# Optimization experiments

Measured on AMD Instinct MI355X. Metric: run time of the kernel, lower is better.

The kernel has to match this reference:

```python
import jax, jax.numpy as jnp
import numpy as np

B, C, N, MAX_OUT = 8, 80, 8192, 100


def setup_inputs() -> dict:
    key = jax.random.key(0)
    k1, k2, k3 = jax.random.split(key, 3)
    xy = jax.random.uniform(k1, (B, N, 2), dtype=jnp.float32)          # top-left corners in [0,1)
    wh = jax.random.uniform(k2, (B, N, 2), dtype=jnp.float32,
                            minval=0.01, maxval=0.2)                    # realistic box sizes
    boxes = jnp.concatenate([xy, xy + wh], axis=-1)                     # [B,N,4] xyxy
    scores = jax.random.uniform(k3, (B, C, N), dtype=jnp.float32)       # [B,C,N]
    return {
        "boxes": boxes,
        "scores": scores,
        "max_output_boxes_per_class": MAX_OUT,
        "iou_threshold": jnp.array([0.5], dtype=jnp.float32),
        "score_threshold": jnp.array([0.5], dtype=jnp.float32),
    }


def _nms_single(boxes, scores, iou_thr, score_thr, max_out):
    """Greedy NMS for one (batch, class): boxes [N,4] xyxy, scores [N].
    Returns [max_out] selected box indices, padded with -1."""
    n = scores.shape[0]
    x1, y1, x2, y2 = boxes[:, 0], boxes[:, 1], boxes[:, 2], boxes[:, 3]
    area = jnp.maximum(x2 - x1, 0.0) * jnp.maximum(y2 - y1, 0.0)
    # score filtering (strictly greater, as in the torch module)
    s0 = jnp.where(scores > score_thr, scores, -jnp.inf)
    iota = jnp.arange(n)

    def body(s, _):
        i = jnp.argmax(s)
        valid = s[i] > -jnp.inf
        bx1, by1, bx2, by2 = boxes[i, 0], boxes[i, 1], boxes[i, 2], boxes[i, 3]
        iw = jnp.maximum(jnp.minimum(x2, bx2) - jnp.maximum(x1, bx1), 0.0)
        ih = jnp.maximum(jnp.minimum(y2, by2) - jnp.maximum(y1, by1), 0.0)
        inter = iw * ih
        union = area + area[i] - inter
        iou = jnp.where(union > 0, inter / union, 0.0)
        # suppress overlapping boxes (iou > thr keeps iou <= thr, matching torchvision.ops.nms)
        suppress = (iou > iou_thr) | (iota == i)
        s_new = jnp.where(suppress, -jnp.inf, s)
        s = jnp.where(valid, s_new, s)
        return s, jnp.where(valid, i, -1)

    _, idxs = jax.lax.scan(body, s0, None, length=max_out)
    return idxs  # [max_out] int32, -1 padded


def reference(boxes, scores, max_output_boxes_per_class, iou_threshold, score_threshold):
    max_out = int(max_output_boxes_per_class)
    iou_thr = iou_threshold[0]
    score_thr = score_threshold[0]
    b, c = scores.shape[0], scores.shape[1]

    # vmap over classes (boxes shared), then over batch
    per_batch = jax.vmap(
        lambda bb, ss: jax.vmap(
            lambda s: _nms_single(bb, s, iou_thr, score_thr, max_out)
        )(ss)
    )
    idxs = per_batch(boxes, scores)  # [B,C,max_out], -1 padded

    valid = idxs >= 0
    bidx = jnp.broadcast_to(jnp.arange(b)[:, None, None], idxs.shape)
    cidx = jnp.broadcast_to(jnp.arange(c)[None, :, None], idxs.shape)
    # [B*C*max_out, 3] rows of (batch, class, box_index); padded rows are (-1,-1,-1).
    triplets = jnp.stack(
        [jnp.where(valid, bidx, -1), jnp.where(valid, cidx, -1), idxs], axis=-1
    ).reshape(-1, 3).astype(jnp.int64)
    return triplets
```

## Files before the change

kernel.cpp:

```cpp
#include <hip/hip_runtime.h>
#include <math.h>
#include <stdint.h>

#define NMS_B 8
#define NMS_C 80
#define NMS_N 8192
#define NMS_MAX_OUT 100
#define BLOCK 512
#define PT 16
#define NBINS 256
#define TARGET 192
#define CAP 256
#define NW 4
#define PADROWS 8

__global__ __launch_bounds__(BLOCK) void nms_jacobi2_kernel(
    const float4* __restrict__ boxes,
    const float*  __restrict__ scores,
    const float*  __restrict__ iou_thr_p,
    const float*  __restrict__ score_thr_p,
    int32_t* __restrict__ out)
{
    const int bc   = blockIdx.x;
    const int b    = bc / NMS_C;
    const int c    = bc % NMS_C;
    const int t    = threadIdx.x;
    const int lane = t & 63;
    const int wv   = t >> 6;

    const float iou_thr   = *iou_thr_p;
    const float score_thr = *score_thr_p;

    __shared__ int      hist[NBINS];
    __shared__ int      cut_bin;
    __shared__ int      gcount;
    __shared__ alignas(16) uint64_t ckey[CAP];
    __shared__ float4   cbox[CAP];
    __shared__ int      cidx[CAP];
    __shared__ float4   sbox[CAP + PADROWS];
    __shared__ int      sidx[CAP];
    __shared__ alignas(16) uint64_t adjT[CAP * NW];

    if (t < NBINS) { hist[t] = 0; ckey[t] = 0; }
    for (int i = t; i < CAP + PADROWS; i += BLOCK)
        sbox[i] = make_float4(0.0f, 0.0f, 0.0f, 0.0f);
    if (t == 0) { cut_bin = 0; gcount = 0; }
    __syncthreads();

    const float* ss = scores + ((size_t)b * NMS_C + c) * NMS_N;
    const float4* ssv = (const float4*)ss;
    float s[PT];
    #pragma unroll
    for (int k4 = 0; k4 < PT / 4; ++k4) {
        float4 v = ssv[k4 * BLOCK + t];
        s[4 * k4 + 0] = v.x; s[4 * k4 + 1] = v.y;
        s[4 * k4 + 2] = v.z; s[4 * k4 + 3] = v.w;
    }
    const float inv_range =
        (score_thr < 1.0f) ? (float)NBINS / (1.0f - score_thr) : 0.0f;
    #pragma unroll
    for (int k = 0; k < PT; ++k) {
        if (s[k] > score_thr) {
            int bin = (int)((s[k] - score_thr) * inv_range);
            bin = bin > NBINS - 1 ? NBINS - 1 : bin;
            atomicAdd(&hist[bin], 1);
        }
    }
    __syncthreads();

    if (wv == 0) {
        int h0 = hist[lane], h1 = hist[64 + lane];
        int h2 = hist[128 + lane], h3 = hist[192 + lane];
        #pragma unroll
        for (int off = 1; off < 64; off <<= 1) {
            const int o0 = __shfl_down(h0, off);
            const int o1 = __shfl_down(h1, off);
            const int o2 = __shfl_down(h2, off);
            const int o3 = __shfl_down(h3, off);
            if (lane + off < 64) { h0 += o0; h1 += o1; h2 += o2; h3 += o3; }
        }
        const int tot1 = __shfl(h1, 0);
        const int tot2 = __shfl(h2, 0);
        const int tot3 = __shfl(h3, 0);
        const int S3 = h3;
        const int S2 = h2 + tot3;
        const int S1 = h1 + tot2 + tot3;
        const int S0 = h0 + tot1 + tot2 + tot3;
        const unsigned long long q3 = __ballot(S3 >= TARGET);
        const unsigned long long q2 = __ballot(S2 >= TARGET);
        const unsigned long long q1 = __ballot(S1 >= TARGET);
        const unsigned long long q0 = __ballot(S0 >= TARGET);
        int cut = 0;
        if      (q3) cut = 192 + 63 - __clzll(q3);
        else if (q2) cut = 128 + 63 - __clzll(q2);
        else if (q1) cut = 64  + 63 - __clzll(q1);
        else if (q0) cut = 63 - __clzll(q0);
        if (lane == 0) cut_bin = cut;
    }
    __syncthreads();
    const int cb = cut_bin;

    const float4* bb = boxes + (size_t)b * NMS_N;
    #pragma unroll
    for (int k = 0; k < PT; ++k) {
        if (s[k] > score_thr) {
            int bin = (int)((s[k] - score_thr) * inv_range);
            bin = bin > NBINS - 1 ? NBINS - 1 : bin;
            if (bin >= cb) {
                int pos = atomicAdd(&gcount, 1);
                if (pos < CAP) {
                    const int k4 = k >> 2, e = k & 3;
                    const int idx = (k4 * BLOCK + t) * 4 + e;
                    cbox[pos] = bb[idx];
                    cidx[pos] = idx;
                    ckey[pos] = ((uint64_t)__float_as_uint(s[k]) << 32) |
                                (uint32_t)(NMS_N - idx);
                }
            }
        }
    }
    __syncthreads();
    const int M = gcount < CAP ? gcount : CAP;

    if (t < CAP) {
        const uint64_t mykey = ckey[t];
        if (mykey != 0) {
            const ulonglong2* kp = (const ulonglong2*)ckey;
            int r = 0;
            #pragma unroll 8
            for (int k = 0; k < CAP / 2; ++k) {
                const ulonglong2 kk = kp[k];
                r += (kk.x > mykey) ? 1 : 0;
                r += (kk.y > mykey) ? 1 : 0;
            }
            sbox[r] = cbox[t];
            sidx[r] = cidx[t];
        }
    } else {
        ulonglong2 z; z.x = 0; z.y = 0;
        ((ulonglong2*)adjT)[t - CAP]       = z;
        ((ulonglong2*)adjT)[t - CAP + 256] = z;
    }
    __syncthreads();

    {
        static const int cw_of[8] = {0, 1, 1, 2, 2, 3, 3, 3};
        const int cw  = cw_of[wv];
        const int Lc0 = (cw + 1) * 64;
        const int Lc  = M < Lc0 ? M : Lc0;
        int rlo, rhi;
        if      (wv == 0) { rlo = 0;   rhi = Lc; }
        else if (wv == 1) { rlo = 0;   rhi = Lc < 64 ? Lc : 64; }
        else if (wv == 2) { rlo = 64;  rhi = Lc; }
        else if (wv == 3) { rlo = 0;   rhi = Lc < 96 ? Lc : 96; }
        else if (wv == 4) { rlo = 96;  rhi = Lc; }
        else {
            const int r1 = (Lc / 3) & ~3;
            const int r2 = (2 * Lc / 3) & ~3;
            if      (wv == 5) { rlo = 0;  rhi = r1; }
            else if (wv == 6) { rlo = r1; rhi = r2; }
            else              { rlo = r2; rhi = Lc; }
        }
        if (rlo < rhi) {
            const int col = cw * 64 + lane;
            const float4 cb4 = sbox[col];
            const float carea = fmaxf(cb4.z - cb4.x, 0.0f) *
                                fmaxf(cb4.w - cb4.y, 0.0f);
            int cur_word = rlo >> 6;
            uint64_t acc = 0;

            float4 p0 = sbox[rlo + 0], p1 = sbox[rlo + 1];
            float4 p2 = sbox[rlo + 2], p3 = sbox[rlo + 3];
            for (int i = rlo; i < rhi; i += 4) {
                const int wblk = i >> 6;
                if (wblk != cur_word) {
                    if (acc) atomicOr((unsigned long long*)&adjT[col * NW + cur_word],
                                      (unsigned long long)acc);
                    acc = 0; cur_word = wblk;
                }
                const float4 q0 = p0, q1 = p1, q2 = p2, q3 = p3;
                p0 = sbox[i + 4]; p1 = sbox[i + 5];
                p2 = sbox[i + 6]; p3 = sbox[i + 7];
                #pragma unroll
                for (int u = 0; u < 4; ++u) {
                    const float4 r4 = (u == 0) ? q0 : (u == 1) ? q1
                                     : (u == 2) ? q2 : q3;
                    const int row = i + u;
                    const float rarea = fmaxf(r4.z - r4.x, 0.0f) *
                                        fmaxf(r4.w - r4.y, 0.0f);
                    const float iw =
                        fmaxf(fminf(cb4.z, r4.z) - fmaxf(cb4.x, r4.x), 0.0f);
                    const float ih =
                        fmaxf(fminf(cb4.w, r4.w) - fmaxf(cb4.y, r4.y), 0.0f);
                    const float inter = iw * ih;
                    const float uni   = carea + rarea - inter;
                    const float iou   = (uni > 0.0f) ? (inter / uni) : 0.0f;
                    const uint64_t bit =
                        (iou > iou_thr && row < rhi) ? 1ull : 0ull;
                    acc |= bit << (row & 63);
                }
            }
            if (acc) atomicOr((unsigned long long*)&adjT[col * NW + cur_word],
                              (unsigned long long)acc);
        }
    }
    __syncthreads();

    int32_t* o = out + (size_t)bc * NMS_MAX_OUT * 3;
    if (t >= 64) return;

    uint64_t adj_[4][4];
    #pragma unroll
    for (int w2 = 0; w2 < 4; ++w2) {
        const int col = w2 * 64 + lane;
        const ulonglong2 lo2 = ((const ulonglong2*)adjT)[col * 2 + 0];
        const ulonglong2 hi2 = ((const ulonglong2*)adjT)[col * 2 + 1];
        adj_[w2][0] = lo2.x; adj_[w2][1] = lo2.y;
        adj_[w2][2] = hi2.x; adj_[w2][3] = hi2.y;
    }
    uint64_t V[4];
    #pragma unroll
    for (int ww = 0; ww < 4; ++ww) {
        const int rem = M - ww * 64;
        V[ww] = (rem >= 64) ? ~0ull : (rem > 0 ? ((1ull << rem) - 1) : 0ull);
    }
    uint64_t A0 = V[0], A1 = V[1], A2 = V[2], A3 = V[3];
    const uint64_t lanelow = (1ull << lane) - 1;

    for (int iter = 0; iter <= CAP; ++iter) {
        bool acc[4];
        #pragma unroll
        for (int w2 = 0; w2 < 4; ++w2) {
            uint64_t rem = 0;
            const uint64_t Aw[4] = {A0, A1, A2, A3};
            #pragma unroll
            for (int ww = 0; ww < 4; ++ww) {
                const uint64_t lm = (ww < w2) ? ~0ull
                                  : (ww == w2 ? lanelow : 0ull);
                rem |= Aw[ww] & lm & adj_[w2][ww];
            }
            acc[w2] = (((V[w2] >> lane) & 1ull) != 0) && (rem == 0);
        }
        const uint64_t N0 = __ballot(acc[0]);
        const uint64_t N1 = __ballot(acc[1]);
        const uint64_t N2 = __ballot(acc[2]);
        const uint64_t N3 = __ballot(acc[3]);
        const bool same = (N0 == A0) && (N1 == A1) && (N2 == A2) && (N3 == A3);
        A0 = N0; A1 = N1; A2 = N2; A3 = N3;
        if (same) break;
    }

    const int pc0 = __popcll(A0), pc1 = __popcll(A1);
    const int pc2 = __popcll(A2), pc3 = __popcll(A3);
    const int total = pc0 + pc1 + pc2 + pc3;
    const int nacc = total < NMS_MAX_OUT ? total : NMS_MAX_OUT;
    const int base[4] = {0, pc0, pc0 + pc1, pc0 + pc1 + pc2};
    #pragma unroll
    for (int w2 = 0; w2 < 4; ++w2) {
        const uint64_t Aw = (w2 == 0) ? A0 : (w2 == 1) ? A1
                          : (w2 == 2) ? A2 : A3;
        if ((Aw >> lane) & 1ull) {
            const int rank = base[w2] + __popcll(Aw & lanelow);
            if (rank < NMS_MAX_OUT) {
                const int col = w2 * 64 + lane;
                o[rank * 3 + 0] = b;
                o[rank * 3 + 1] = c;
                o[rank * 3 + 2] = sidx[col];
            }
        }
    }
    for (int m = nacc + t; m < NMS_MAX_OUT; m += 64) {
        o[m * 3 + 0] = -1;
        o[m * 3 + 1] = -1;
        o[m * 3 + 2] = -1;
    }
}

extern "C" void kernel_launch(void* const* d_in, const int* in_sizes, int n_in,
                              void* d_out, int out_size, void* d_ws, size_t ws_size,
                              hipStream_t stream) {
    (void)in_sizes; (void)n_in; (void)d_ws; (void)ws_size; (void)out_size;
    const float4* boxes  = (const float4*)d_in[0];
    const float*  scores = (const float*)d_in[1];
    const float*  iou_thr   = (const float*)d_in[3];
    const float*  score_thr = (const float*)d_in[4];
    int32_t* out = (int32_t*)d_out;

    dim3 grid(NMS_B * NMS_C);
    dim3 block(BLOCK);
    hipLaunchKernelGGL(nms_jacobi2_kernel, grid, block, 0, stream,
                       boxes, scores, iou_thr, score_thr, out);
}
```

Before: 111.8 us.

## Flatten IoU work across waves, precompute box areas, cache histogram bins

The IoU adjacency build now treats all column-word/row pairs as one flat work list and splits it evenly across the 8 waves, replacing the hand-tuned wave-to-column mapping. Box areas are computed once at sort time into a shared array and loaded, not recomputed per pair. Histogram bin indices are packed into registers during the first pass so the compaction pass does not recompute them. This adds a small shared array and a per-wave loop over column groups, which may increase atomicOr traffic at segment boundaries.

Result: no change. 109.7 us (-1.9%).

```diff
diff --git a/kernel.cpp b/kernel.cpp
--- a/kernel.cpp
+++ b/kernel.cpp
@@ -14,7 +14,7 @@
 #define NW 4
 #define PADROWS 8
 
-__global__ __launch_bounds__(BLOCK) void nms_jacobi2_kernel(
+__global__ __launch_bounds__(BLOCK) void nms_flat_kernel(
     const float4* __restrict__ boxes,
     const float*  __restrict__ scores,
     const float*  __restrict__ iou_thr_p,
@@ -38,12 +38,15 @@
     __shared__ float4   cbox[CAP];
     __shared__ int      cidx[CAP];
     __shared__ float4   sbox[CAP + PADROWS];
+    __shared__ float    sar[CAP + PADROWS];
     __shared__ int      sidx[CAP];
     __shared__ alignas(16) uint64_t adjT[CAP * NW];
 
     if (t < NBINS) { hist[t] = 0; ckey[t] = 0; }
-    for (int i = t; i < CAP + PADROWS; i += BLOCK)
+    for (int i = t; i < CAP + PADROWS; i += BLOCK) {
         sbox[i] = make_float4(0.0f, 0.0f, 0.0f, 0.0f);
+        sar[i]  = 0.0f;
+    }
     if (t == 0) { cut_bin = 0; gcount = 0; }
     __syncthreads();
 
@@ -58,12 +61,14 @@
     }
     const float inv_range =
         (score_thr < 1.0f) ? (float)NBINS / (1.0f - score_thr) : 0.0f;
+    uint32_t pk[PT / 4] = {0, 0, 0, 0};
     #pragma unroll
     for (int k = 0; k < PT; ++k) {
         if (s[k] > score_thr) {
             int bin = (int)((s[k] - score_thr) * inv_range);
             bin = bin > NBINS - 1 ? NBINS - 1 : bin;
             atomicAdd(&hist[bin], 1);
+            pk[k >> 2] |= (uint32_t)bin << ((k & 3) * 8);
         }
     }
     __syncthreads();
@@ -104,13 +109,12 @@
     #pragma unroll
     for (int k = 0; k < PT; ++k) {
         if (s[k] > score_thr) {
-            int bin = (int)((s[k] - score_thr) * inv_range);
-            bin = bin > NBINS - 1 ? NBINS - 1 : bin;
+            const int bin = (pk[k >> 2] >> ((k & 3) * 8)) & 255;
             if (bin >= cb) {
                 int pos = atomicAdd(&gcount, 1);
                 if (pos < CAP) {
-                    const int k4 = k >> 2, e = k & 3;
-                    const int idx = (k4 * BLOCK + t) * 4 + e;
+                    const int k4 = k >> 2, el = k & 3;
+                    const int idx = (k4 * BLOCK + t) * 4 + el;
                     cbox[pos] = bb[idx];
                     cidx[pos] = idx;
                     ckey[pos] = ((uint64_t)__float_as_uint(s[k]) << 32) |
@@ -133,7 +137,9 @@
                 r += (kk.x > mykey) ? 1 : 0;
                 r += (kk.y > mykey) ? 1 : 0;
             }
-            sbox[r] = cbox[t];
+            const float4 v = cbox[t];
+            sbox[r] = v;
+            sar[r]  = fmaxf(v.z - v.x, 0.0f) * fmaxf(v.w - v.y, 0.0f);
             sidx[r] = cidx[t];
         }
     } else {
@@ -144,50 +150,58 @@
     __syncthreads();
 
     {
-        static const int cw_of[8] = {0, 1, 1, 2, 2, 3, 3, 3};
-        const int cw  = cw_of[wv];
-        const int Lc0 = (cw + 1) * 64;
-        const int Lc  = M < Lc0 ? M : Lc0;
-        int rlo, rhi;
-        if      (wv == 0) { rlo = 0;   rhi = Lc; }
-        else if (wv == 1) { rlo = 0;   rhi = Lc < 64 ? Lc : 64; }
-        else if (wv == 2) { rlo = 64;  rhi = Lc; }
-        else if (wv == 3) { rlo = 0;   rhi = Lc < 96 ? Lc : 96; }
-        else if (wv == 4) { rlo = 96;  rhi = Lc; }
-        else {
-            const int r1 = (Lc / 3) & ~3;
-            const int r2 = (2 * Lc / 3) & ~3;
-            if      (wv == 5) { rlo = 0;  rhi = r1; }
-            else if (wv == 6) { rlo = r1; rhi = r2; }
-            else              { rlo = r2; rhi = Lc; }
-        }
-        if (rlo < rhi) {
+        const int L0c = M <  64 ? M :  64;
+        const int L1c = M < 128 ? M : 128;
+        const int L2c = M < 192 ? M : 192;
+        const int L3c = M;
+        int cum[5];
+        cum[0] = 0;
+        cum[1] = L0c;
+        cum[2] = L0c + L1c;
+        cum[3] = L0c + L1c + L2c;
+        cum[4] = L0c + L1c + L2c + L3c;
+        const int G  = cum[4];
+        const int g0 = ((wv * G) >> 3) & ~3;
+        const int g1 = (wv == 7) ? G : (((wv + 1) * G) >> 3) & ~3;
+
+        for (int cw = 0; cw < 4; ++cw) {
+            const int a = g0 > cum[cw] ? g0 : cum[cw];
+            const int e = g1 < cum[cw + 1] ? g1 : cum[cw + 1];
+            if (a >= e) continue;
+            const int rlo = a - cum[cw];
+            const int rhi = e - cum[cw];
             const int col = cw * 64 + lane;
-            const float4 cb4 = sbox[col];
-            const float carea = fmaxf(cb4.z - cb4.x, 0.0f) *
-                                fmaxf(cb4.w - cb4.y, 0.0f);
+            const float4 cb4  = sbox[col];
+            const float carea = sar[col];
+
             int cur_word = rlo >> 6;
             uint64_t acc = 0;
-
             float4 p0 = sbox[rlo + 0], p1 = sbox[rlo + 1];
             float4 p2 = sbox[rlo + 2], p3 = sbox[rlo + 3];
+            float  e0 = sar[rlo + 0], e1 = sar[rlo + 1];
+            float  e2 = sar[rlo + 2], e3 = sar[rlo + 3];
+
             for (int i = rlo; i < rhi; i += 4) {
                 const int wblk = i >> 6;
                 if (wblk != cur_word) {
-                    if (acc) atomicOr((unsigned long long*)&adjT[col * NW + cur_word],
-                                      (unsigned long long)acc);
+                    if (acc) atomicOr(
+                        (unsigned long long*)&adjT[col * NW + cur_word],
+                        (unsigned long long)acc);
                     acc = 0; cur_word = wblk;
                 }
                 const float4 q0 = p0, q1 = p1, q2 = p2, q3 = p3;
+                const float  f0 = e0, f1 = e1, f2 = e2, f3 = e3;
                 p0 = sbox[i + 4]; p1 = sbox[i + 5];
                 p2 = sbox[i + 6]; p3 = sbox[i + 7];
+                e0 = sar[i + 4]; e1 = sar[i + 5];
+                e2 = sar[i + 6]; e3 = sar[i + 7];
                 #pragma unroll
                 for (int u = 0; u < 4; ++u) {
                     const float4 r4 = (u == 0) ? q0 : (u == 1) ? q1
                                      : (u == 2) ? q2 : q3;
+                    const float rarea = (u == 0) ? f0 : (u == 1) ? f1
+                                      : (u == 2) ? f2 : f3;
                     const int row = i + u;
-                    const float rarea = fmaxf(r4.z - r4.x, 0.0f) *
-                                        fmaxf(r4.w - r4.y, 0.0f);
                     const float iw =
                         fmaxf(fminf(cb4.z, r4.z) - fmaxf(cb4.x, r4.x), 0.0f);
                     const float ih =
@@ -200,8 +214,9 @@
                     acc |= bit << (row & 63);
                 }
             }
-            if (acc) atomicOr((unsigned long long*)&adjT[col * NW + cur_word],
-                              (unsigned long long)acc);
+            if (acc) atomicOr(
+                (unsigned long long*)&adjT[col * NW + cur_word],
+                (unsigned long long)acc);
         }
     }
     __syncthreads();
@@ -288,6 +303,6 @@
 
     dim3 grid(NMS_B * NMS_C);
     dim3 block(BLOCK);
-    hipLaunchKernelGGL(nms_jacobi2_kernel, grid, block, 0, stream,
+    hipLaunchKernelGGL(nms_flat_kernel, grid, block, 0, stream,
                        boxes, scores, iou_thr, score_thr, out);
 }
```
